# Kernel tuning notes

Hardware: AMD Instinct MI355X
Metric: run time of the kernel (lower is better)

Reference implementation:

```python
import jax, jax.numpy as jnp
import numpy as np

B, S, D, F, H, E = 2, 1024, 1024, 4096, 16, 8
EPS = 1e-5


def _layernorm(x, w, b):
    m = jnp.mean(x, -1, keepdims=True)
    v = jnp.var(x, -1, keepdims=True)
    return (x - m) * jax.lax.rsqrt(v + EPS) * w + b


def _rope(x):
    # rotary embedding applied over full embed dim (split-half convention)
    b, s, d = x.shape
    half = d // 2
    inv = 1.0 / (10000.0 ** (jnp.arange(half, dtype=jnp.float32) / half))
    ang = jnp.arange(s, dtype=jnp.float32)[:, None] * inv[None, :]  # [S, half]
    cos, sin = jnp.cos(ang), jnp.sin(ang)
    x1, x2 = x[..., :half], x[..., half:]
    return jnp.concatenate([x1 * cos - x2 * sin, x1 * sin + x2 * cos], -1)


def setup_inputs() -> dict:
    key = jax.random.key(0)
    ks = jax.random.split(key, 9)
    sc = 0.02
    return {
        "x": jax.random.normal(ks[0], (B, S, D), jnp.float32),
        "ln1_w": jnp.ones((D,), jnp.float32),
        "ln1_b": jnp.zeros((D,), jnp.float32),
        "ln2_w": jnp.ones((D,), jnp.float32),
        "ln2_b": jnp.zeros((D,), jnp.float32),
        "w_qkv": jax.random.normal(ks[1], (3 * D, D), jnp.float32) * sc,
        "b_qkv": jnp.zeros((3 * D,), jnp.float32),
        "w_out": jax.random.normal(ks[2], (D, D), jnp.float32) * sc,
        "b_out": jnp.zeros((D,), jnp.float32),
        "w_router": jax.random.normal(ks[3], (D, E), jnp.float32) * sc,
        "wi": jax.random.normal(ks[4], (E, D, F), jnp.float32) * sc,  # per-expert wi (no bias)
        "wo": jax.random.normal(ks[5], (E, F // 2, D), jnp.float32) * sc,  # swiglu halves ffn dim
    }


def reference(x, ln1_w, ln1_b, ln2_w, ln2_b, w_qkv, b_qkv, w_out, b_out, w_router, wi, wo):
    # ---- pre-norm self-attention block ----
    residual = x
    h = _layernorm(x, ln1_w, ln1_b)
    h = _rope(h)
    qkv = h @ w_qkv.T + b_qkv  # [B,S,3D]
    q, k, v = jnp.split(qkv, 3, axis=-1)
    hd = D // H
    to_heads = lambda t: t.reshape(B, S, H, hd).transpose(0, 2, 1, 3)
    q, k, v = to_heads(q), to_heads(k), to_heads(v)
    scale = 1.0 / np.sqrt(hd).astype(np.float32)
    att = jax.nn.softmax(jnp.einsum('bhqd,bhkd->bhqk', q, k) * scale, axis=-1)
    o = jnp.einsum('bhqk,bhkd->bhqd', att, v).transpose(0, 2, 1, 3).reshape(B, S, D)
    o = o @ w_out.T + b_out
    x = residual + o  # attn dropout is identity at eval

    # ---- pre-norm sparse MoE FFN block ----
    residual = x
    h = _layernorm(x, ln2_w, ln2_b)
    # top-1 router in float32
    logits = h.astype(jnp.float32) @ w_router  # [B,S,E]
    probs = jax.nn.softmax(logits, axis=-1)
    mask = jax.nn.one_hot(jnp.argmax(probs, -1), E, dtype=h.dtype)  # expert_mask
    gate = probs.astype(h.dtype) * mask  # router_probs * expert_mask, [B,S,E]
    # dense all-expert compute, masked combine (same math as gather/scatter loop)
    hid = jnp.einsum('bsd,edf->bsef', h, wi)  # [B,S,E,F]
    a, g = jnp.split(hid, 2, axis=-1)
    act = jax.nn.silu(a) * g  # SwiGLU, [B,S,E,F/2]
    y = jnp.einsum('bsef,efd,bse->bsd', act, wo, gate)
    x = residual + y
    return x, logits
```

## Files before the change

kernel.cpp:

```cpp
#include <hip/hip_runtime.h>
#include <hip/hip_bf16.h>
#include <math.h>

#define BB 2
#define SS 1024
#define DD 1024
#define FF 4096
#define HH 16
#define EE 8
#define MM (BB*SS)
#define MAX_TILES 24
#define MAX_TILES2 40

typedef __attribute__((ext_vector_type(8))) short bf16x8;
typedef __attribute__((ext_vector_type(8))) short s16x8;
typedef __attribute__((ext_vector_type(4))) float f32x4;

#define OFF_WIT  ((size_t)0)
#define OFF_WOT  ((size_t)67108864)
#define OFF_WQH  ((size_t)100663296)
#define OFF_WQL  ((size_t)106954752)
#define OFF_WOH  ((size_t)113246208)
#define OFF_WOL  ((size_t)115343360)
#define OFF_H1H  ((size_t)117440512)
#define OFF_H1L  ((size_t)121634816)
#define OFF_QKV  ((size_t)125829120)
#define OFF_OH   ((size_t)150994944)
#define OFF_OL   ((size_t)155189248)
#define OFF_X2   ((size_t)159383552)
#define OFF_H2B  ((size_t)167772160)
#define OFF_ACT  ((size_t)171966464)
#define OFF_GATE ((size_t)180879360)
#define OFF_EID  ((size_t)180887552)
#define OFF_PERM ((size_t)180895744)
#define OFF_CNT  ((size_t)180903936)
#define OFF_FILL ((size_t)180903968)
#define OFF_NT   ((size_t)180904000)
#define OFF_TE   ((size_t)180904192)
#define OFF_TS   ((size_t)180904320)
#define OFF_TR   ((size_t)180904448)
#define OFF_TE2  ((size_t)180904576)
#define OFF_TS2  ((size_t)180904768)
#define OFF_TR2  ((size_t)180904960)
#define OFF_NT2  ((size_t)180905152)
#define OFF_KSH  OFF_WQH
#define OFF_KSL  (OFF_WQH + 4194304)
#define OFF_VTH  OFF_H1H
#define OFF_VTL  OFF_H1L

__device__ __forceinline__ void gload16(const void* g, void* l) {
    __builtin_amdgcn_global_load_lds(
        (const __attribute__((address_space(1))) unsigned int*)g,
        (__attribute__((address_space(3))) unsigned int*)l, 16, 0, 0);
}

__device__ __forceinline__ short bfh(float v) {
    __hip_bfloat16 h = __float2bfloat16(v);
    return *(short*)&h;
}
__device__ __forceinline__ float bf2f(short s) {
    __hip_bfloat16 h = *(__hip_bfloat16*)&s;
    return __bfloat162float(h);
}

__device__ __forceinline__ void split_write(float v, __hip_bfloat16* hp, __hip_bfloat16* lp, size_t idx) {
    __hip_bfloat16 h = __float2bfloat16(v);
    hp[idx] = h;
    lp[idx] = __float2bfloat16(v - __bfloat162float(h));
}

__device__ __forceinline__ void tcvt64_body(const float* __restrict__ in, __hip_bfloat16* __restrict__ out,
                                            int R, int C, int r0, int c0, float* tile ) {
    int t = threadIdx.x;
    {
        int ri = t >> 2, cj = (t & 3) * 16;
        const float* ip = &in[(size_t)(r0 + ri) * C + c0 + cj];
#pragma unroll
        for (int k = 0; k < 4; ++k) {
            float4 v = *(const float4*)(ip + k * 4);
            tile[ri * 65 + cj + k * 4 + 0] = v.x;
            tile[ri * 65 + cj + k * 4 + 1] = v.y;
            tile[ri * 65 + cj + k * 4 + 2] = v.z;
            tile[ri * 65 + cj + k * 4 + 3] = v.w;
        }
    }
    __syncthreads();
    {
        int co = t >> 2, rj = (t & 3) * 16;
        bf16x8 v8a, v8b;
#pragma unroll
        for (int q = 0; q < 8; ++q) v8a[q] = bfh(tile[(rj + q) * 65 + co]);
#pragma unroll
        for (int q = 0; q < 8; ++q) v8b[q] = bfh(tile[(rj + 8 + q) * 65 + co]);
        __hip_bfloat16* op = &out[(size_t)(c0 + co) * R + r0 + rj];
        *(bf16x8*)op = v8a;
        *(bf16x8*)(op + 8) = v8b;
    }
}

__global__ void k_phase0(const float* __restrict__ x, const float* __restrict__ ln1w,
                         const float* __restrict__ ln1b,
                         __hip_bfloat16* __restrict__ h1H, __hip_bfloat16* __restrict__ h1L,
                         const float* __restrict__ w_qkv, __hip_bfloat16* __restrict__ wqH,
                         __hip_bfloat16* __restrict__ wqL,
                         const float* __restrict__ w_out, __hip_bfloat16* __restrict__ woH,
                         __hip_bfloat16* __restrict__ woL) {
    __shared__ __align__(16) float smem[1032];
    int bid = blockIdx.x, t = threadIdx.x;
    if (bid < 2048) {
        int m = bid, s = m & (SS - 1);
        float* row = smem;
        float* red = smem + 1024;
        const float* xp = x + (size_t)m * DD;
        float sum = 0.f, sumsq = 0.f;
#pragma unroll
        for (int l = 0; l < 4; ++l) {
            int i = t + l * 256;
            float v = xp[i];
            row[i] = v;
            sum += v; sumsq += v * v;
        }
#pragma unroll
        for (int off = 32; off; off >>= 1) {
            sum   += __shfl_xor(sum, off);
            sumsq += __shfl_xor(sumsq, off);
        }
        int wid = t >> 6, lane = t & 63;
        if (lane == 0) { red[wid] = sum; red[4 + wid] = sumsq; }
        __syncthreads();
        sum   = red[0] + red[1] + red[2] + red[3];
        sumsq = red[4] + red[5] + red[6] + red[7];
        float mean = sum * (1.f / DD);
        float var  = sumsq * (1.f / DD) - mean * mean;
        float rstd = rsqrtf(var + 1e-5f);
        size_t base = (size_t)m * DD;
        const float kln = logf(10000.f) / 512.f;
#pragma unroll
        for (int l = 0; l < 2; ++l) {
            int i = t + l * 256;
            float n1 = (row[i]       - mean) * rstd * ln1w[i]       + ln1b[i];
            float n2 = (row[i + 512] - mean) * rstd * ln1w[i + 512] + ln1b[i + 512];
            float inv = expf(-(float)i * kln);
            float ang = (float)s * inv;
            float c = cosf(ang), sn = sinf(ang);
            split_write(n1 * c - n2 * sn,  h1H, h1L, base + i);
            split_write(n1 * sn + n2 * c, h1H, h1L, base + i + 512);
        }
    } else if (bid < 5120) {
        int idx = (bid - 2048) * 256 + t;
        float4 v = ((const float4*)w_qkv)[idx];
        split_write(v.x, wqH, wqL, (size_t)idx * 4 + 0);
        split_write(v.y, wqH, wqL, (size_t)idx * 4 + 1);
        split_write(v.z, wqH, wqL, (size_t)idx * 4 + 2);
        split_write(v.w, wqH, wqL, (size_t)idx * 4 + 3);
    } else {
        int idx = (bid - 5120) * 256 + t;
        float4 v = ((const float4*)w_out)[idx];
        split_write(v.x, woH, woL, (size_t)idx * 4 + 0);
        split_write(v.y, woH, woL, (size_t)idx * 4 + 1);
        split_write(v.z, woH, woL, (size_t)idx * 4 + 2);
        split_write(v.w, woH, woL, (size_t)idx * 4 + 3);
    }
}

__global__ void k_qkv_mega(const __hip_bfloat16* __restrict__ Ah, const __hip_bfloat16* __restrict__ Al,
                           const __hip_bfloat16* __restrict__ Bh, const __hip_bfloat16* __restrict__ Bl,
                           const float* __restrict__ bias, float* __restrict__ Cf,
                           const float* __restrict__ wi, __hip_bfloat16* __restrict__ wiT) {
    __shared__ __align__(16) char smem[24576];
    int bid = blockIdx.x;
    const int t = threadIdx.x;
    if (bid < 768) {
        const int N = 3072, K = DD;
        short* AsH = (short*)smem;
        short* AsL = (short*)(smem + 4096);
        short* BsH = (short*)(smem + 8192);
        short* BsL = (short*)(smem + 16384);
        int m0 = (bid / 24) * 64, n0 = (bid % 24) * 128;
        const int w = t >> 6, lane = t & 63;
        const int sid = w * 64 + lane;
        const int g = lane >> 4, r16 = lane & 15;

        f32x4 acc[4][2] = {};

        for (int k0 = 0; k0 < K; k0 += 32) {
            {
                int rrow = sid >> 2, sl = sid & 3;
                int slog = sl ^ ((rrow >> 1) & 3);
                size_t lbase = (size_t)(w * 64) * 8;
                size_t gaoff = (size_t)(m0 + rrow) * K + k0 + slog * 8;
                gload16(Ah + gaoff, &AsH[lbase]);
                gload16(Al + gaoff, &AsL[lbase]);
            }
#pragma unroll
            for (int j = 0; j < 2; ++j) {
                int id = j * 256 + sid;
                int rrow = id >> 2, sl = id & 3;
                int slog = sl ^ ((rrow >> 1) & 3);
                size_t lbase = (size_t)(j * 256 + w * 64) * 8;
                size_t gboff = (size_t)(n0 + rrow) * K + k0 + slog * 8;
                gload16(Bh + gboff, &BsH[lbase]);
                gload16(Bl + gboff, &BsL[lbase]);
            }
            __syncthreads();
            bf16x8 ah[4], al[4], bh[2], bl[2];
#pragma unroll
            for (int i = 0; i < 4; ++i) {
                int ra = i * 16 + r16;
                int pa = g ^ ((ra >> 1) & 3);
                ah[i] = *(const bf16x8*)&AsH[ra * 32 + pa * 8];
                al[i] = *(const bf16x8*)&AsL[ra * 32 + pa * 8];
            }
#pragma unroll
            for (int n = 0; n < 2; ++n) {
                int rb = w * 32 + n * 16 + r16;
                int pb = g ^ ((rb >> 1) & 3);
                bh[n] = *(const bf16x8*)&BsH[rb * 32 + pb * 8];
                bl[n] = *(const bf16x8*)&BsL[rb * 32 + pb * 8];
            }
#pragma unroll
            for (int i = 0; i < 4; ++i)
#pragma unroll
                for (int n = 0; n < 2; ++n) {
                    acc[i][n] = __builtin_amdgcn_mfma_f32_16x16x32_bf16(ah[i], bh[n], acc[i][n], 0, 0, 0);
                    acc[i][n] = __builtin_amdgcn_mfma_f32_16x16x32_bf16(ah[i], bl[n], acc[i][n], 0, 0, 0);
                    acc[i][n] = __builtin_amdgcn_mfma_f32_16x16x32_bf16(al[i], bh[n], acc[i][n], 0, 0, 0);
                }
            __syncthreads();
        }

#pragma unroll
        for (int i = 0; i < 4; ++i) {
#pragma unroll
            for (int n = 0; n < 2; ++n) {
                int col = n0 + w * 32 + n * 16 + r16;
#pragma unroll
                for (int q = 0; q < 4; ++q) {
                    int r = m0 + i * 16 + g * 4 + q;
                    Cf[(size_t)r * N + col] = acc[i][n][q] + bias[col];
                }
            }
        }
    } else {
        int j = bid - 768;
        int e = j >> 10, rem = j & 1023;
        int ry = rem >> 6, cx = rem & 63;
        tcvt64_body(wi + (size_t)e * DD * FF, wiT + (size_t)e * DD * FF,
                    1024, 4096, ry * 64, cx * 64, (float*)smem);
    }
}

__global__ void k_oproj64(const __hip_bfloat16* __restrict__ Ah, const __hip_bfloat16* __restrict__ Al,
                          const __hip_bfloat16* __restrict__ Bh, const __hip_bfloat16* __restrict__ Bl,
                          const float* __restrict__ bias, const float* __restrict__ addsrc,
                          float* __restrict__ Cf, int* __restrict__ zero17) {
    __shared__ __align__(16) short AsH[64 * 32];
    __shared__ __align__(16) short AsL[64 * 32];
    __shared__ __align__(16) short BsH[128 * 32];
    __shared__ __align__(16) short BsL[128 * 32];
    const int N = DD, K = DD;
    int bid = blockIdx.x;
    int m0 = (bid >> 3) * 64, n0 = (bid & 7) * 128;
    const int t = threadIdx.x;
    if (bid == 0 && t < 17) zero17[t] = 0;
    const int w = t >> 6, lane = t & 63;
    const int sid = w * 64 + lane;
    const int g = lane >> 4, r16 = lane & 15;

    f32x4 acc[4][2] = {};

    for (int k0 = 0; k0 < K; k0 += 32) {
        {
            int rrow = sid >> 2, sl = sid & 3;
            int slog = sl ^ ((rrow >> 1) & 3);
            size_t lbase = (size_t)(w * 64) * 8;
            size_t gaoff = (size_t)(m0 + rrow) * K + k0 + slog * 8;
            gload16(Ah + gaoff, &AsH[lbase]);
            gload16(Al + gaoff, &AsL[lbase]);
        }
#pragma unroll
        for (int j = 0; j < 2; ++j) {
            int id = j * 256 + sid;
            int rrow = id >> 2, sl = id & 3;
            int slog = sl ^ ((rrow >> 1) & 3);
            size_t lbase = (size_t)(j * 256 + w * 64) * 8;
            size_t gboff = (size_t)(n0 + rrow) * K + k0 + slog * 8;
            gload16(Bh + gboff, &BsH[lbase]);
            gload16(Bl + gboff, &BsL[lbase]);
        }
        __syncthreads();
        bf16x8 ah[4], al[4], bh[2], bl[2];
#pragma unroll
        for (int i = 0; i < 4; ++i) {
            int ra = i * 16 + r16;
            int pa = g ^ ((ra >> 1) & 3);
            ah[i] = *(const bf16x8*)&AsH[ra * 32 + pa * 8];
            al[i] = *(const bf16x8*)&AsL[ra * 32 + pa * 8];
        }
#pragma unroll
        for (int n = 0; n < 2; ++n) {
            int rb = w * 32 + n * 16 + r16;
            int pb = g ^ ((rb >> 1) & 3);
            bh[n] = *(const bf16x8*)&BsH[rb * 32 + pb * 8];
            bl[n] = *(const bf16x8*)&BsL[rb * 32 + pb * 8];
        }
#pragma unroll
        for (int i = 0; i < 4; ++i)
#pragma unroll
            for (int n = 0; n < 2; ++n) {
                acc[i][n] = __builtin_amdgcn_mfma_f32_16x16x32_bf16(ah[i], bh[n], acc[i][n], 0, 0, 0);
                acc[i][n] = __builtin_amdgcn_mfma_f32_16x16x32_bf16(ah[i], bl[n], acc[i][n], 0, 0, 0);
                acc[i][n] = __builtin_amdgcn_mfma_f32_16x16x32_bf16(al[i], bh[n], acc[i][n], 0, 0, 0);
            }
        __syncthreads();
    }

#pragma unroll
    for (int i = 0; i < 4; ++i) {
#pragma unroll
        for (int n = 0; n < 2; ++n) {
            int col = n0 + w * 32 + n * 16 + r16;
#pragma unroll
            for (int q = 0; q < 4; ++q) {
                int r = m0 + i * 16 + g * 4 + q;
                Cf[(size_t)r * N + col] =
                    acc[i][n][q] + bias[col] + addsrc[(size_t)r * N + col];
            }
        }
    }
}

__global__ void k_moe_up(const __hip_bfloat16* __restrict__ A,
                         const __hip_bfloat16* __restrict__ Bt,
                         __hip_bfloat16* __restrict__ act,
                         const int* __restrict__ perm,
                         const int* __restrict__ te, const int* __restrict__ ts,
                         const int* __restrict__ tr, const int* __restrict__ ntl,
                         const float* __restrict__ wo, __hip_bfloat16* __restrict__ woT) {
    __shared__ __align__(16) char smem[17408];
    int bid = blockIdx.x;
    const int t = threadIdx.x;
    if (bid >= 768) {
        int j = bid - 768;
        int e = j >> 9, rem = j & 511;
        int ry = rem >> 4, cx = rem & 15;
        tcvt64_body(wo + (size_t)e * 2048 * 1024, woT + (size_t)e * 2048 * 1024,
                    2048, 1024, ry * 64, cx * 64, (float*)smem);
        return;
    }
    short* As = (short*)smem;
    short* Bs = (short*)(smem + 8192);
    int* permS = (int*)(smem + 16384);
    int tile = bid / 32;
    if (tile >= *ntl) return;
    int e = te[tile], rs = ts[tile], rows = tr[tile];
    if (t < 128) permS[t] = (t < rows) ? perm[rs + t] : 0;
    __syncthreads();
    int c0 = (bid & 31) * 64;
    const int w = t >> 6, lane = t & 63;
    const int wr = w >> 1, wc = w & 1;
    const int sid = w * 64 + lane;
    const int g = lane >> 4, r16 = lane & 15;

    const __hip_bfloat16* Bp = Bt + (size_t)e * FF * DD;

    f32x4 acc[4][4] = {};

    for (int k0 = 0; k0 < DD; k0 += 32) {
#pragma unroll
        for (int j = 0; j < 2; ++j) {
            int id = j * 256 + sid;
            int rrow = id >> 2, sl = id & 3;
            int slog = sl ^ ((rrow >> 1) & 3);
            size_t lbase = (size_t)(j * 256 + w * 64) * 8;
            gload16(A + (size_t)permS[rrow] * DD + k0 + slog * 8, &As[lbase]);
            int q = rrow >> 4, rr = rrow & 15;
            int wrow = c0 + (q >> 2) * 32 + ((q & 3) >> 1) * 16 + rr + (q & 1) * 2048;
            gload16(Bp + (size_t)wrow * DD + k0 + slog * 8, &Bs[lbase]);
        }
        __syncthreads();
        bf16x8 af[4], bfr[4];
#pragma unroll
        for (int i = 0; i < 4; ++i) {
            int ra = wr * 64 + i * 16 + r16;
            int pa = g ^ ((ra >> 1) & 3);
            af[i] = *(const bf16x8*)&As[ra * 32 + pa * 8];
            int rb = wc * 64 + i * 16 + r16;
            int pb = g ^ ((rb >> 1) & 3);
            bfr[i] = *(const bf16x8*)&Bs[rb * 32 + pb * 8];
        }
#pragma unroll
        for (int i = 0; i < 4; ++i)
#pragma unroll
            for (int n = 0; n < 4; ++n)
                acc[i][n] = __builtin_amdgcn_mfma_f32_16x16x32_bf16(af[i], bfr[n], acc[i][n], 0, 0, 0);
        __syncthreads();
    }

#pragma unroll
    for (int i = 0; i < 4; ++i) {
#pragma unroll
        for (int p2 = 0; p2 < 2; ++p2) {
            int col = c0 + wc * 32 + p2 * 16 + r16;
#pragma unroll
            for (int q = 0; q < 4; ++q) {
                int r = wr * 64 + i * 16 + g * 4 + q;
                if (r < rows) {
                    float a  = acc[i][2 * p2][q];
                    float gv = acc[i][2 * p2 + 1][q];
                    act[(size_t)(rs + r) * 2048 + col] =
                        __float2bfloat16((a / (1.f + expf(-a))) * gv);
                }
            }
        }
    }
}

__global__ void k_moe_dn(const __hip_bfloat16* __restrict__ A,
                         const __hip_bfloat16* __restrict__ Bt,
                         const float* __restrict__ addsrc, float* __restrict__ Cf,
                         const int* __restrict__ perm,
                         const int* __restrict__ te2, const int* __restrict__ ts2,
                         const int* __restrict__ tr2, const int* __restrict__ ntl2,
                         const float* __restrict__ gate) {
    __shared__ __align__(16) short As[64 * 32];
    __shared__ __align__(16) short Bs[128 * 32];
    __shared__ int permS[64];
    int tile = blockIdx.y;
    if (tile >= *ntl2) return;
    int e = te2[tile], rs = ts2[tile], rows = tr2[tile];
    const int t = threadIdx.x;
    if (t < 64) permS[t] = (t < rows) ? perm[rs + t] : 0;
    __syncthreads();
    int n0 = blockIdx.x * 128;
    const int w = t >> 6, lane = t & 63;
    const int sid = w * 64 + lane;
    const int g = lane >> 4, r16 = lane & 15;
    const int K = FF / 2;

    const __hip_bfloat16* Bp = Bt + (size_t)e * DD * (FF / 2);

    f32x4 acc[4][2] = {};

    for (int k0 = 0; k0 < K; k0 += 32) {
        {
            int rrow = sid >> 2, sl = sid & 3;
            int slog = sl ^ ((rrow >> 1) & 3);
            size_t lbase = (size_t)(w * 64) * 8;
            gload16(A + (size_t)(rs + rrow) * K + k0 + slog * 8, &As[lbase]);
        }
#pragma unroll
        for (int j = 0; j < 2; ++j) {
            int id = j * 256 + sid;
            int rrow = id >> 2, sl = id & 3;
            int slog = sl ^ ((rrow >> 1) & 3);
            size_t lbase = (size_t)(j * 256 + w * 64) * 8;
            gload16(Bp + (size_t)(n0 + rrow) * K + k0 + slog * 8, &Bs[lbase]);
        }
        __syncthreads();
        bf16x8 af[4], bfr[2];
#pragma unroll
        for (int i = 0; i < 4; ++i) {
            int ra = i * 16 + r16;
            int pa = g ^ ((ra >> 1) & 3);
            af[i] = *(const bf16x8*)&As[ra * 32 + pa * 8];
        }
#pragma unroll
        for (int n = 0; n < 2; ++n) {
            int rb = w * 32 + n * 16 + r16;
            int pb = g ^ ((rb >> 1) & 3);
            bfr[n] = *(const bf16x8*)&Bs[rb * 32 + pb * 8];
        }
#pragma unroll
        for (int i = 0; i < 4; ++i)
#pragma unroll
            for (int n = 0; n < 2; ++n)
                acc[i][n] = __builtin_amdgcn_mfma_f32_16x16x32_bf16(af[i], bfr[n], acc[i][n], 0, 0, 0);
        __syncthreads();
    }

#pragma unroll
    for (int i = 0; i < 4; ++i) {
#pragma unroll
        for (int n = 0; n < 2; ++n) {
            int col = n0 + w * 32 + n * 16 + r16;
#pragma unroll
            for (int q = 0; q < 4; ++q) {
                int r = i * 16 + g * 4 + q;
                if (r >= rows) continue;
                int tok = permS[r];
                Cf[(size_t)tok * DD + col] = addsrc[(size_t)tok * DD + col] + gate[tok] * acc[i][n][q];
            }
        }
    }
}

__global__ void k_prep(const float* __restrict__ qkv, short* __restrict__ KH, short* __restrict__ KL,
                       short* __restrict__ VH, short* __restrict__ VL) {
    __shared__ float tile[64][65];
    int b = blockIdx.z, h = blockIdx.y, s0 = blockIdx.x * 64;
    int t = threadIdx.x;
    int row = t >> 2, c0 = (t & 3) * 16;
    const float* kp = qkv + (size_t)(b * SS + s0 + row) * 3072 + 1024 + h * 64 + c0;
    const float* vp = kp + 1024;
    {
        size_t krow = ((size_t)(b * HH + h) * SS + s0 + row) * 64;
        int key = (s0 + row) & 7;
#pragma unroll
        for (int g2 = 0; g2 < 2; ++g2) {
            s16x8 hv, lv;
#pragma unroll
            for (int j = 0; j < 8; ++j) {
                float v = kp[g2 * 8 + j];
                short hh = bfh(v);
                hv[j] = hh; lv[j] = bfh(v - bf2f(hh));
            }
            int p = ((c0 >> 3) + g2) ^ key;
            *(s16x8*)&KH[krow + p * 8] = hv;
            *(s16x8*)&KL[krow + p * 8] = lv;
        }
    }
#pragma unroll
    for (int j = 0; j < 16; ++j) tile[row][c0 + j] = vp[j];
    __syncthreads();
    {
        int d = t >> 2, sc = (t & 3) * 16;
        size_t vrow = ((size_t)(b * HH + h) * 64 + d) * SS + s0;
        int key = d & 7;
#pragma unroll
        for (int g2 = 0; g2 < 2; ++g2) {
            s16x8 hv, lv;
#pragma unroll
            for (int j = 0; j < 8; ++j) {
                float v = tile[sc + g2 * 8 + j][d];
                short hh = bfh(v);
                hv[j] = hh; lv[j] = bfh(v - bf2f(hh));
            }
            int p = ((sc >> 3) + g2) ^ key;
            *(s16x8*)&VH[vrow + p * 8] = hv;
            *(s16x8*)&VL[vrow + p * 8] = lv;
        }
    }
}

#define LDP 72
__global__ __launch_bounds__(512, 4)
void k_attn_mfma(const float* __restrict__ qkv,
                 const short* __restrict__ KH, const short* __restrict__ KL,
                 const short* __restrict__ VH, const short* __restrict__ VL,
                 __hip_bfloat16* __restrict__ ohi, __hip_bfloat16* __restrict__ olo) {
    __shared__ __align__(16) short Ks[64 * 64], Kl2[64 * 64], Vs[64 * 64], Vl2[64 * 64];
    __shared__ __align__(16) short PhS[8][16 * LDP], PlS[8][16 * LDP];
    int id = blockIdx.x;
    int xcd = id & 7, slot = id >> 3;
    int bh = xcd * 4 + (slot >> 3);
    int q0 = (slot & 7) * 128;
    int b = bh >> 4, h = bh & 15;
    int t = threadIdx.x;
    int w = t >> 6, lane = t & 63;
    int g = lane >> 4, r16 = lane & 15;
    int srow = t >> 3, sslot = t & 7;

    const size_t kbase = ((size_t)bh * SS) * 64;
    const size_t vbase = ((size_t)bh * 64) * SS;

    bf16x8 qfh[2], qfl[2];
    {
        const float* qp = qkv + (size_t)(b * SS + q0 + w * 16 + r16) * 3072 + h * 64;
#pragma unroll
        for (int ks = 0; ks < 2; ++ks) {
            float vv[8];
            *(float4*)&vv[0] = *(const float4*)(qp + ks * 32 + g * 8);
            *(float4*)&vv[4] = *(const float4*)(qp + ks * 32 + g * 8 + 4);
#pragma unroll
            for (int j = 0; j < 8; ++j) {
                float sv = vv[j] * 0.125f;
                short hh = bfh(sv);
                qfh[ks][j] = hh;
                qfl[ks][j] = bfh(sv - bf2f(hh));
            }
        }
    }

    float mrun[4], lrun[4];
    f32x4 oacc[4] = {};
#pragma unroll
    for (int q = 0; q < 4; ++q) { mrun[q] = -1e30f; lrun[q] = 0.f; }

    for (int k0 = 0; k0 < SS; k0 += 64) {
        gload16(KH + kbase + (size_t)(k0 + srow) * 64 + sslot * 8, &Ks[w * 512]);
        gload16(KL + kbase + (size_t)(k0 + srow) * 64 + sslot * 8, &Kl2[w * 512]);
        gload16(VH + vbase + (size_t)srow * SS + k0 + sslot * 8,   &Vs[w * 512]);
        gload16(VL + vbase + (size_t)srow * SS + k0 + sslot * 8,   &Vl2[w * 512]);
        __syncthreads();

        f32x4 accs[4] = {};
#pragma unroll
        for (int ks = 0; ks < 2; ++ks) {
            bf16x8 kfh[4], kfl[4];
#pragma unroll
            for (int n = 0; n < 4; ++n) {
                int rb = n * 16 + r16;
                int p = (ks * 4 + g) ^ (r16 & 7);
                kfh[n] = *(const bf16x8*)&Ks[rb * 64 + p * 8];
                kfl[n] = *(const bf16x8*)&Kl2[rb * 64 + p * 8];
            }
            __builtin_amdgcn_s_setprio(1);
#pragma unroll
            for (int n = 0; n < 4; ++n) {
                accs[n] = __builtin_amdgcn_mfma_f32_16x16x32_bf16(qfh[ks], kfh[n], accs[n], 0, 0, 0);
                accs[n] = __builtin_amdgcn_mfma_f32_16x16x32_bf16(qfh[ks], kfl[n], accs[n], 0, 0, 0);
                accs[n] = __builtin_amdgcn_mfma_f32_16x16x32_bf16(qfl[ks], kfh[n], accs[n], 0, 0, 0);
            }
            __builtin_amdgcn_s_setprio(0);
        }

        float mn[4], corr[4], psum[4];
#pragma unroll
        for (int q = 0; q < 4; ++q) {
            float m = fmaxf(fmaxf(accs[0][q], accs[1][q]), fmaxf(accs[2][q], accs[3][q]));
            m = fmaxf(m, __shfl_xor(m, 1));
            m = fmaxf(m, __shfl_xor(m, 2));
            m = fmaxf(m, __shfl_xor(m, 4));
            m = fmaxf(m, __shfl_xor(m, 8));
            mn[q] = fmaxf(mrun[q], m);
            corr[q] = expf(mrun[q] - mn[q]);
            mrun[q] = mn[q];
            psum[q] = 0.f;
        }
#pragma unroll
        for (int n = 0; n < 4; ++n)
#pragma unroll
            for (int q = 0; q < 4; ++q) {
                float p = expf(accs[n][q] - mn[q]);
                psum[q] += p;
                short ph = bfh(p);
                PhS[w][(g * 4 + q) * LDP + n * 16 + r16] = ph;
                PlS[w][(g * 4 + q) * LDP + n * 16 + r16] = bfh(p - bf2f(ph));
            }
#pragma unroll
        for (int q = 0; q < 4; ++q) {
            psum[q] += __shfl_xor(psum[q], 1);
            psum[q] += __shfl_xor(psum[q], 2);
            psum[q] += __shfl_xor(psum[q], 4);
            psum[q] += __shfl_xor(psum[q], 8);
            lrun[q] = lrun[q] * corr[q] + psum[q];
#pragma unroll
            for (int n = 0; n < 4; ++n) oacc[n][q] *= corr[q];
        }

#pragma unroll
        for (int ks = 0; ks < 2; ++ks) {
            bf16x8 vfh[4], vfl[4];
#pragma unroll
            for (int n = 0; n < 4; ++n) {
                int rb = n * 16 + r16;
                int p = (ks * 4 + g) ^ (r16 & 7);
                vfh[n] = *(const bf16x8*)&Vs[rb * 64 + p * 8];
                vfl[n] = *(const bf16x8*)&Vl2[rb * 64 + p * 8];
            }
            bf16x8 pfh = *(const bf16x8*)&PhS[w][r16 * LDP + ks * 32 + g * 8];
            bf16x8 pfl = *(const bf16x8*)&PlS[w][r16 * LDP + ks * 32 + g * 8];
            __builtin_amdgcn_s_setprio(1);
#pragma unroll
            for (int n = 0; n < 4; ++n) {
                oacc[n] = __builtin_amdgcn_mfma_f32_16x16x32_bf16(pfh, vfh[n], oacc[n], 0, 0, 0);
                oacc[n] = __builtin_amdgcn_mfma_f32_16x16x32_bf16(pfh, vfl[n], oacc[n], 0, 0, 0);
                oacc[n] = __builtin_amdgcn_mfma_f32_16x16x32_bf16(pfl, vfh[n], oacc[n], 0, 0, 0);
            }
            __builtin_amdgcn_s_setprio(0);
        }
        __syncthreads();
    }

    float invl[4];
#pragma unroll
    for (int q = 0; q < 4; ++q) invl[q] = 1.f / lrun[q];
#pragma unroll
    for (int n = 0; n < 4; ++n) {
        int col = h * 64 + n * 16 + r16;
#pragma unroll
        for (int q = 0; q < 4; ++q) {
            int rowg = b * SS + q0 + w * 16 + g * 4 + q;
            split_write(oacc[n][q] * invl[q], ohi, olo, (size_t)rowg * DD + col);
        }
    }
}

__global__ void k_ln2_router(const float* __restrict__ x2, const float* __restrict__ w,
                             const float* __restrict__ b, const float* __restrict__ wr,
                             __hip_bfloat16* __restrict__ h2b, float* __restrict__ logits,
                             float* __restrict__ gate, int* __restrict__ eid,
                             int* __restrict__ counts) {
    int m = blockIdx.x, t = threadIdx.x;
    __shared__ float red[8];
    __shared__ float racc[4][8];
    const float* xp = x2 + (size_t)m * DD;
    float v[4];
    float sum = 0.f, sumsq = 0.f;
#pragma unroll
    for (int l = 0; l < 4; ++l) {
        v[l] = xp[t + l * 256];
        sum += v[l]; sumsq += v[l] * v[l];
    }
#pragma unroll
    for (int off = 32; off; off >>= 1) {
        sum   += __shfl_xor(sum, off);
        sumsq += __shfl_xor(sumsq, off);
    }
    int wid = t >> 6, lane = t & 63;
    if (lane == 0) { red[wid] = sum; red[4 + wid] = sumsq; }
    __syncthreads();
    sum   = red[0] + red[1] + red[2] + red[3];
    sumsq = red[4] + red[5] + red[6] + red[7];
    float mean = sum * (1.f / DD);
    float var  = sumsq * (1.f / DD) - mean * mean;
    float rstd = rsqrtf(var + 1e-5f);
    float acc[EE] = {};
#pragma unroll
    for (int l = 0; l < 4; ++l) {
        int i = t + l * 256;
        float hv = (v[l] - mean) * rstd * w[i] + b[i];
        h2b[(size_t)m * DD + i] = __float2bfloat16(hv);
        const float* wp = wr + (size_t)i * EE;
#pragma unroll
        for (int n = 0; n < EE; ++n) acc[n] += hv * wp[n];
    }
#pragma unroll
    for (int off = 32; off; off >>= 1)
#pragma unroll
        for (int n = 0; n < EE; ++n) acc[n] += __shfl_xor(acc[n], off);
    if (lane == 0)
#pragma unroll
        for (int n = 0; n < EE; ++n) racc[wid][n] = acc[n];
    __syncthreads();
    if (t == 0) {
        float lg[EE];
#pragma unroll
        for (int n = 0; n < EE; ++n) lg[n] = racc[0][n] + racc[1][n] + racc[2][n] + racc[3][n];
        float mx = lg[0]; int best = 0;
#pragma unroll
        for (int n = 1; n < EE; ++n) if (lg[n] > mx) { mx = lg[n]; best = n; }
        float den = 0.f;
#pragma unroll
        for (int n = 0; n < EE; ++n) den += expf(lg[n] - mx);
        gate[m] = 1.f / den;
        eid[m] = best;
        atomicAdd(&counts[best], 1);
#pragma unroll
        for (int n = 0; n < EE; ++n) logits[(size_t)m * EE + n] = lg[n];
    }
}

__global__ void k_offscatter(const int* __restrict__ counts,
                             int* __restrict__ te, int* __restrict__ ts, int* __restrict__ tr,
                             int* __restrict__ ntl,
                             int* __restrict__ te2, int* __restrict__ ts2, int* __restrict__ tr2,
                             int* __restrict__ ntl2,
                             const int* __restrict__ eid,
                             int* __restrict__ fill, int* __restrict__ perm) {
    __shared__ int soffs[EE];
    int t = threadIdx.x;
    if (t == 0) {
        int off = 0, nt = 0, nt2 = 0;
        for (int e = 0; e < EE; ++e) {
            soffs[e] = off;
            int c = counts[e];
            for (int t0 = 0; t0 < c; t0 += 128) {
                te[nt] = e; ts[nt] = off + t0; tr[nt] = (c - t0 < 128) ? (c - t0) : 128; ++nt;
            }
            for (int t0 = 0; t0 < c; t0 += 64) {
                te2[nt2] = e; ts2[nt2] = off + t0; tr2[nt2] = (c - t0 < 64) ? (c - t0) : 64; ++nt2;
            }
            off += c;
        }
        *ntl = nt;
        *ntl2 = nt2;
    }
    __syncthreads();
#pragma unroll
    for (int tok = t; tok < MM; tok += 1024) {
        int e = eid[tok];
        int pos = soffs[e] + atomicAdd(&fill[e], 1);
        perm[pos] = tok;
    }
}

extern "C" void kernel_launch(void* const* d_in, const int* in_sizes, int n_in,
                              void* d_out, int out_size, void* d_ws, size_t ws_size,
                              hipStream_t stream) {
    const float* x     = (const float*)d_in[0];
    const float* ln1w  = (const float*)d_in[1];
    const float* ln1b  = (const float*)d_in[2];
    const float* ln2w  = (const float*)d_in[3];
    const float* ln2b  = (const float*)d_in[4];
    const float* w_qkv = (const float*)d_in[5];
    const float* b_qkv = (const float*)d_in[6];
    const float* w_out = (const float*)d_in[7];
    const float* b_out = (const float*)d_in[8];
    const float* w_rtr = (const float*)d_in[9];
    const float* wi    = (const float*)d_in[10];
    const float* wo    = (const float*)d_in[11];
    float* out = (float*)d_out;

    char* wsb = (char*)d_ws;
    __hip_bfloat16* wiT  = (__hip_bfloat16*)(wsb + OFF_WIT);
    __hip_bfloat16* woT  = (__hip_bfloat16*)(wsb + OFF_WOT);
    __hip_bfloat16* wqH  = (__hip_bfloat16*)(wsb + OFF_WQH);
    __hip_bfloat16* wqL  = (__hip_bfloat16*)(wsb + OFF_WQL);
    __hip_bfloat16* woH  = (__hip_bfloat16*)(wsb + OFF_WOH);
    __hip_bfloat16* woL  = (__hip_bfloat16*)(wsb + OFF_WOL);
    __hip_bfloat16* h1H  = (__hip_bfloat16*)(wsb + OFF_H1H);
    __hip_bfloat16* h1L  = (__hip_bfloat16*)(wsb + OFF_H1L);
    float*          qkvF = (float*)(wsb + OFF_QKV);
    __hip_bfloat16* oH   = (__hip_bfloat16*)(wsb + OFF_OH);
    __hip_bfloat16* oL   = (__hip_bfloat16*)(wsb + OFF_OL);
    float*          x2F  = (float*)(wsb + OFF_X2);
    __hip_bfloat16* h2B  = (__hip_bfloat16*)(wsb + OFF_H2B);
    __hip_bfloat16* actB = (__hip_bfloat16*)(wsb + OFF_ACT);
    short* KSH = (short*)(wsb + OFF_KSH);
    short* KSL = (short*)(wsb + OFF_KSL);
    short* VTH = (short*)(wsb + OFF_VTH);
    short* VTL = (short*)(wsb + OFF_VTL);
    float* gate = (float*)(wsb + OFF_GATE);
    int* eid    = (int*)(wsb + OFF_EID);
    int* perm   = (int*)(wsb + OFF_PERM);
    int* counts = (int*)(wsb + OFF_CNT);
    int* fill   = (int*)(wsb + OFF_FILL);
    int* ntl    = (int*)(wsb + OFF_NT);
    int* te     = (int*)(wsb + OFF_TE);
    int* tsx    = (int*)(wsb + OFF_TS);
    int* trx    = (int*)(wsb + OFF_TR);
    int* te2    = (int*)(wsb + OFF_TE2);
    int* ts2    = (int*)(wsb + OFF_TS2);
    int* tr2    = (int*)(wsb + OFF_TR2);
    int* ntl2   = (int*)(wsb + OFF_NT2);

    k_phase0<<<6144, 256, 0, stream>>>(x, ln1w, ln1b, h1H, h1L, w_qkv, wqH, wqL,
                                       w_out, woH, woL);
    k_qkv_mega<<<8960, 256, 0, stream>>>(h1H, h1L, wqH, wqL, b_qkv, qkvF, wi, wiT);
    k_prep<<<dim3(SS / 64, HH, BB), 256, 0, stream>>>(qkvF, KSH, KSL, VTH, VTL);
    k_attn_mfma<<<256, 512, 0, stream>>>(qkvF, KSH, KSL, VTH, VTL, oH, oL);
    k_oproj64<<<256, 256, 0, stream>>>(oH, oL, woH, woL, b_out, x, x2F, counts);
    k_ln2_router<<<MM, 256, 0, stream>>>(x2F, ln2w, ln2b, w_rtr, h2B,
                                         out + (size_t)MM * DD, gate, eid, counts);
    k_offscatter<<<1, 1024, 0, stream>>>(counts, te, tsx, trx, ntl,
                                         te2, ts2, tr2, ntl2, eid, fill, perm);
    k_moe_up<<<768 + 4096, 256, 0, stream>>>(h2B, wiT, actB, perm, te, tsx, trx, ntl,
                                             wo, woT);
    k_moe_dn<<<dim3(DD / 128, MAX_TILES2), 256, 0, stream>>>(
        actB, woT, x2F, out, perm, te2, ts2, tr2, ntl2, gate);
}
```

Measured before the change: 320.3 us.

## Move expert weight transposes into attention kernel and XCD-swizzle QKV GEMM

The wi and wo transpose-to-bf16 blocks move out of the QKV GEMM and MoE-up kernels and become extra blocks of the attention kernel, two 256-thread tiles per 512-thread block. The attention kernel is only 256 blocks, so the transpose work is meant to fill idle CUs alongside it. The QKV GEMM becomes a plain 768-block kernel whose tile mapping groups N tiles per XCD for L2 reuse. In exchange, attention now reserves a larger shared buffer (68 KB), which may lower its occupancy.

```diff
diff --git a/kernel.cpp b/kernel.cpp
--- a/kernel.cpp
+++ b/kernel.cpp
@@ -70,8 +70,7 @@
 }
 
 __device__ __forceinline__ void tcvt64_body(const float* __restrict__ in, __hip_bfloat16* __restrict__ out,
-                                            int R, int C, int r0, int c0, float* tile ) {
-    int t = threadIdx.x;
+                                            int R, int C, int r0, int c0, float* tile , int t) {
     {
         int ri = t >> 2, cj = (t & 3) * 16;
         const float* ip = &in[(size_t)(r0 + ri) * C + c0 + cj];
@@ -163,90 +162,83 @@
     }
 }
 
-__global__ void k_qkv_mega(const __hip_bfloat16* __restrict__ Ah, const __hip_bfloat16* __restrict__ Al,
-                           const __hip_bfloat16* __restrict__ Bh, const __hip_bfloat16* __restrict__ Bl,
-                           const float* __restrict__ bias, float* __restrict__ Cf,
-                           const float* __restrict__ wi, __hip_bfloat16* __restrict__ wiT) {
-    __shared__ __align__(16) char smem[24576];
+__global__ void k_qkv(const __hip_bfloat16* __restrict__ Ah, const __hip_bfloat16* __restrict__ Al,
+                      const __hip_bfloat16* __restrict__ Bh, const __hip_bfloat16* __restrict__ Bl,
+                      const float* __restrict__ bias, float* __restrict__ Cf) {
+    __shared__ __align__(16) short AsH[64 * 32];
+    __shared__ __align__(16) short AsL[64 * 32];
+    __shared__ __align__(16) short BsH[128 * 32];
+    __shared__ __align__(16) short BsL[128 * 32];
+    const int N = 3072, K = DD;
     int bid = blockIdx.x;
+    int xcd = bid & 7, idx = bid >> 3;
+    int nt = xcd + (idx >> 5) * 8;
+    int mt = idx & 31;
+    int m0 = mt * 64, n0 = nt * 128;
     const int t = threadIdx.x;
-    if (bid < 768) {
-        const int N = 3072, K = DD;
-        short* AsH = (short*)smem;
-        short* AsL = (short*)(smem + 4096);
-        short* BsH = (short*)(smem + 8192);
-        short* BsL = (short*)(smem + 16384);
-        int m0 = (bid / 24) * 64, n0 = (bid % 24) * 128;
-        const int w = t >> 6, lane = t & 63;
-        const int sid = w * 64 + lane;
-        const int g = lane >> 4, r16 = lane & 15;
-
-        f32x4 acc[4][2] = {};
-
-        for (int k0 = 0; k0 < K; k0 += 32) {
-            {
-                int rrow = sid >> 2, sl = sid & 3;
-                int slog = sl ^ ((rrow >> 1) & 3);
-                size_t lbase = (size_t)(w * 64) * 8;
-                size_t gaoff = (size_t)(m0 + rrow) * K + k0 + slog * 8;
-                gload16(Ah + gaoff, &AsH[lbase]);
-                gload16(Al + gaoff, &AsL[lbase]);
-            }
-#pragma unroll
-            for (int j = 0; j < 2; ++j) {
-                int id = j * 256 + sid;
-                int rrow = id >> 2, sl = id & 3;
-                int slog = sl ^ ((rrow >> 1) & 3);
-                size_t lbase = (size_t)(j * 256 + w * 64) * 8;
-                size_t gboff = (size_t)(n0 + rrow) * K + k0 + slog * 8;
-                gload16(Bh + gboff, &BsH[lbase]);
-                gload16(Bl + gboff, &BsL[lbase]);
-            }
-            __syncthreads();
-            bf16x8 ah[4], al[4], bh[2], bl[2];
-#pragma unroll
-            for (int i = 0; i < 4; ++i) {
-                int ra = i * 16 + r16;
-                int pa = g ^ ((ra >> 1) & 3);
-                ah[i] = *(const bf16x8*)&AsH[ra * 32 + pa * 8];
-                al[i] = *(const bf16x8*)&AsL[ra * 32 + pa * 8];
-            }
+    const int w = t >> 6, lane = t & 63;
+    const int sid = w * 64 + lane;
+    const int g = lane >> 4, r16 = lane & 15;
+
+    f32x4 acc[4][2] = {};
+
+    for (int k0 = 0; k0 < K; k0 += 32) {
+        {
+            int rrow = sid >> 2, sl = sid & 3;
+            int slog = sl ^ ((rrow >> 1) & 3);
+            size_t lbase = (size_t)(w * 64) * 8;
+            size_t gaoff = (size_t)(m0 + rrow) * K + k0 + slog * 8;
+            gload16(Ah + gaoff, &AsH[lbase]);
+            gload16(Al + gaoff, &AsL[lbase]);
+        }
+#pragma unroll
+        for (int j = 0; j < 2; ++j) {
+            int id = j * 256 + sid;
+            int rrow = id >> 2, sl = id & 3;
+            int slog = sl ^ ((rrow >> 1) & 3);
+            size_t lbase = (size_t)(j * 256 + w * 64) * 8;
+            size_t gboff = (size_t)(n0 + rrow) * K + k0 + slog * 8;
+            gload16(Bh + gboff, &BsH[lbase]);
+            gload16(Bl + gboff, &BsL[lbase]);
+        }
+        __syncthreads();
+        bf16x8 ah[4], al[4], bh[2], bl[2];
+#pragma unroll
+        for (int i = 0; i < 4; ++i) {
+            int ra = i * 16 + r16;
+            int pa = g ^ ((ra >> 1) & 3);
+            ah[i] = *(const bf16x8*)&AsH[ra * 32 + pa * 8];
+            al[i] = *(const bf16x8*)&AsL[ra * 32 + pa * 8];
+        }
+#pragma unroll
+        for (int n = 0; n < 2; ++n) {
+            int rb = w * 32 + n * 16 + r16;
+            int pb = g ^ ((rb >> 1) & 3);
+            bh[n] = *(const bf16x8*)&BsH[rb * 32 + pb * 8];
+            bl[n] = *(const bf16x8*)&BsL[rb * 32 + pb * 8];
+        }
+#pragma unroll
+        for (int i = 0; i < 4; ++i)
 #pragma unroll
             for (int n = 0; n < 2; ++n) {
-                int rb = w * 32 + n * 16 + r16;
-                int pb = g ^ ((rb >> 1) & 3);
-                bh[n] = *(const bf16x8*)&BsH[rb * 32 + pb * 8];
-                bl[n] = *(const bf16x8*)&BsL[rb * 32 + pb * 8];
-            }
-#pragma unroll
-            for (int i = 0; i < 4; ++i)
-#pragma unroll
-                for (int n = 0; n < 2; ++n) {
-                    acc[i][n] = __builtin_amdgcn_mfma_f32_16x16x32_bf16(ah[i], bh[n], acc[i][n], 0, 0, 0);
-                    acc[i][n] = __builtin_amdgcn_mfma_f32_16x16x32_bf16(ah[i], bl[n], acc[i][n], 0, 0, 0);
-                    acc[i][n] = __builtin_amdgcn_mfma_f32_16x16x32_bf16(al[i], bh[n], acc[i][n], 0, 0, 0);
-                }
-            __syncthreads();
-        }
-
-#pragma unroll
-        for (int i = 0; i < 4; ++i) {
-#pragma unroll
-            for (int n = 0; n < 2; ++n) {
-                int col = n0 + w * 32 + n * 16 + r16;
-#pragma unroll
-                for (int q = 0; q < 4; ++q) {
-                    int r = m0 + i * 16 + g * 4 + q;
-                    Cf[(size_t)r * N + col] = acc[i][n][q] + bias[col];
-                }
-            }
-        }
-    } else {
-        int j = bid - 768;
-        int e = j >> 10, rem = j & 1023;
-        int ry = rem >> 6, cx = rem & 63;
-        tcvt64_body(wi + (size_t)e * DD * FF, wiT + (size_t)e * DD * FF,
-                    1024, 4096, ry * 64, cx * 64, (float*)smem);
+                acc[i][n] = __builtin_amdgcn_mfma_f32_16x16x32_bf16(ah[i], bh[n], acc[i][n], 0, 0, 0);
+                acc[i][n] = __builtin_amdgcn_mfma_f32_16x16x32_bf16(ah[i], bl[n], acc[i][n], 0, 0, 0);
+                acc[i][n] = __builtin_amdgcn_mfma_f32_16x16x32_bf16(al[i], bh[n], acc[i][n], 0, 0, 0);
+            }
+        __syncthreads();
+    }
+
+#pragma unroll
+    for (int i = 0; i < 4; ++i) {
+#pragma unroll
+        for (int n = 0; n < 2; ++n) {
+            int col = n0 + w * 32 + n * 16 + r16;
+#pragma unroll
+            for (int q = 0; q < 4; ++q) {
+                int r = m0 + i * 16 + g * 4 + q;
+                Cf[(size_t)r * N + col] = acc[i][n][q] + bias[col];
+            }
+        }
     }
 }
 
@@ -335,28 +327,17 @@
                          __hip_bfloat16* __restrict__ act,
                          const int* __restrict__ perm,
                          const int* __restrict__ te, const int* __restrict__ ts,
-                         const int* __restrict__ tr, const int* __restrict__ ntl,
-                         const float* __restrict__ wo, __hip_bfloat16* __restrict__ woT) {
-    __shared__ __align__(16) char smem[17408];
-    int bid = blockIdx.x;
-    const int t = threadIdx.x;
-    if (bid >= 768) {
-        int j = bid - 768;
-        int e = j >> 9, rem = j & 511;
-        int ry = rem >> 4, cx = rem & 15;
-        tcvt64_body(wo + (size_t)e * 2048 * 1024, woT + (size_t)e * 2048 * 1024,
-                    2048, 1024, ry * 64, cx * 64, (float*)smem);
-        return;
-    }
-    short* As = (short*)smem;
-    short* Bs = (short*)(smem + 8192);
-    int* permS = (int*)(smem + 16384);
-    int tile = bid / 32;
+                         const int* __restrict__ tr, const int* __restrict__ ntl) {
+    __shared__ __align__(16) short As[128 * 32];
+    __shared__ __align__(16) short Bs[128 * 32];
+    __shared__ int permS[128];
+    int tile = blockIdx.y;
     if (tile >= *ntl) return;
     int e = te[tile], rs = ts[tile], rows = tr[tile];
+    const int t = threadIdx.x;
     if (t < 128) permS[t] = (t < rows) ? perm[rs + t] : 0;
     __syncthreads();
-    int c0 = (bid & 31) * 64;
+    int c0 = blockIdx.x * 64;
     const int w = t >> 6, lane = t & 63;
     const int wr = w >> 1, wc = w & 1;
     const int sid = w * 64 + lane;
@@ -545,13 +526,38 @@
 
 #define LDP 72
 __global__ __launch_bounds__(512, 4)
-void k_attn_mfma(const float* __restrict__ qkv,
+void k_attn_mega(const float* __restrict__ qkv,
                  const short* __restrict__ KH, const short* __restrict__ KL,
                  const short* __restrict__ VH, const short* __restrict__ VL,
-                 __hip_bfloat16* __restrict__ ohi, __hip_bfloat16* __restrict__ olo) {
-    __shared__ __align__(16) short Ks[64 * 64], Kl2[64 * 64], Vs[64 * 64], Vl2[64 * 64];
-    __shared__ __align__(16) short PhS[8][16 * LDP], PlS[8][16 * LDP];
+                 __hip_bfloat16* __restrict__ ohi, __hip_bfloat16* __restrict__ olo,
+                 const float* __restrict__ wi, __hip_bfloat16* __restrict__ wiT,
+                 const float* __restrict__ wo, __hip_bfloat16* __restrict__ woT) {
+    __shared__ __align__(16) char smem[69632];
     int id = blockIdx.x;
+    if (id >= 256) {
+        int t512 = threadIdx.x;
+        int half = t512 >> 8, t = t512 & 255;
+        float* tile = (float*)(smem + half * 33280 / 2 * 2);
+        tile = (float*)(smem + half * 16640);
+        if (id < 4352) {
+            int gidx = (id - 256) * 2 + half;
+            int e = gidx >> 10, rem = gidx & 1023;
+            int ry = rem >> 6, cx = rem & 63;
+            tcvt64_body(wi + (size_t)e * DD * FF, wiT + (size_t)e * DD * FF,
+                        1024, 4096, ry * 64, cx * 64, tile, t);
+        } else {
+            int gidx = (id - 4352) * 2 + half;
+            int e = gidx >> 9, rem = gidx & 511;
+            int ry = rem >> 4, cx = rem & 15;
+            tcvt64_body(wo + (size_t)e * 2048 * 1024, woT + (size_t)e * 2048 * 1024,
+                        2048, 1024, ry * 64, cx * 64, tile, t);
+        }
+        return;
+    }
+    short* Ks  = (short*)smem;
+    short* Kl2 = (short*)(smem + 8192);
+    short* Vs  = (short*)(smem + 16384);
+    short* Vl2 = (short*)(smem + 24576);
     int xcd = id & 7, slot = id >> 3;
     int bh = xcd * 4 + (slot >> 3);
     int q0 = (slot & 7) * 128;
@@ -560,6 +566,8 @@
     int w = t >> 6, lane = t & 63;
     int g = lane >> 4, r16 = lane & 15;
     int srow = t >> 3, sslot = t & 7;
+    short* PhS = (short*)(smem + 32768 + w * 2304);
+    short* PlS = (short*)(smem + 51200 + w * 2304);
 
     const size_t kbase = ((size_t)bh * SS) * 64;
     const size_t vbase = ((size_t)bh * 64) * SS;
@@ -588,10 +596,10 @@
     for (int q = 0; q < 4; ++q) { mrun[q] = -1e30f; lrun[q] = 0.f; }
 
     for (int k0 = 0; k0 < SS; k0 += 64) {
-        gload16(KH + kbase + (size_t)(k0 + srow) * 64 + sslot * 8, &Ks[w * 512]);
-        gload16(KL + kbase + (size_t)(k0 + srow) * 64 + sslot * 8, &Kl2[w * 512]);
-        gload16(VH + vbase + (size_t)srow * SS + k0 + sslot * 8,   &Vs[w * 512]);
-        gload16(VL + vbase + (size_t)srow * SS + k0 + sslot * 8,   &Vl2[w * 512]);
+        gload16(KH + kbase + (size_t)(k0 + srow) * 64 + sslot * 8, Ks  + w * 512);
+        gload16(KL + kbase + (size_t)(k0 + srow) * 64 + sslot * 8, Kl2 + w * 512);
+        gload16(VH + vbase + (size_t)srow * SS + k0 + sslot * 8,   Vs  + w * 512);
+        gload16(VL + vbase + (size_t)srow * SS + k0 + sslot * 8,   Vl2 + w * 512);
         __syncthreads();
 
         f32x4 accs[4] = {};
@@ -635,8 +643,8 @@
                 float p = expf(accs[n][q] - mn[q]);
                 psum[q] += p;
                 short ph = bfh(p);
-                PhS[w][(g * 4 + q) * LDP + n * 16 + r16] = ph;
-                PlS[w][(g * 4 + q) * LDP + n * 16 + r16] = bfh(p - bf2f(ph));
+                PhS[(g * 4 + q) * LDP + n * 16 + r16] = ph;
+                PlS[(g * 4 + q) * LDP + n * 16 + r16] = bfh(p - bf2f(ph));
             }
 #pragma unroll
         for (int q = 0; q < 4; ++q) {
@@ -659,8 +667,8 @@
                 vfh[n] = *(const bf16x8*)&Vs[rb * 64 + p * 8];
                 vfl[n] = *(const bf16x8*)&Vl2[rb * 64 + p * 8];
             }
-            bf16x8 pfh = *(const bf16x8*)&PhS[w][r16 * LDP + ks * 32 + g * 8];
-            bf16x8 pfl = *(const bf16x8*)&PlS[w][r16 * LDP + ks * 32 + g * 8];
+            bf16x8 pfh = *(const bf16x8*)&PhS[r16 * LDP + ks * 32 + g * 8];
+            bf16x8 pfl = *(const bf16x8*)&PlS[r16 * LDP + ks * 32 + g * 8];
             __builtin_amdgcn_s_setprio(1);
 #pragma unroll
             for (int n = 0; n < 4; ++n) {
@@ -838,16 +846,16 @@
 
     k_phase0<<<6144, 256, 0, stream>>>(x, ln1w, ln1b, h1H, h1L, w_qkv, wqH, wqL,
                                        w_out, woH, woL);
-    k_qkv_mega<<<8960, 256, 0, stream>>>(h1H, h1L, wqH, wqL, b_qkv, qkvF, wi, wiT);
+    k_qkv<<<768, 256, 0, stream>>>(h1H, h1L, wqH, wqL, b_qkv, qkvF);
     k_prep<<<dim3(SS / 64, HH, BB), 256, 0, stream>>>(qkvF, KSH, KSL, VTH, VTL);
-    k_attn_mfma<<<256, 512, 0, stream>>>(qkvF, KSH, KSL, VTH, VTL, oH, oL);
+    k_attn_mega<<<6400, 512, 0, stream>>>(qkvF, KSH, KSL, VTH, VTL, oH, oL,
+                                          wi, wiT, wo, woT);
     k_oproj64<<<256, 256, 0, stream>>>(oH, oL, woH, woL, b_out, x, x2F, counts);
     k_ln2_router<<<MM, 256, 0, stream>>>(x2F, ln2w, ln2b, w_rtr, h2B,
                                          out + (size_t)MM * DD, gate, eid, counts);
     k_offscatter<<<1, 1024, 0, stream>>>(counts, te, tsx, trx, ntl,
                                          te2, ts2, tr2, ntl2, eid, fill, perm);
-    k_moe_up<<<768 + 4096, 256, 0, stream>>>(h2B, wiT, actB, perm, te, tsx, trx, ntl,
-                                             wo, woT);
+    k_moe_up<<<dim3(32, MAX_TILES), 256, 0, stream>>>(h2B, wiT, actB, perm, te, tsx, trx, ntl);
     k_moe_dn<<<dim3(DD / 128, MAX_TILES2), 256, 0, stream>>>(
         actB, woT, x2F, out, perm, te2, ts2, tr2, ntl2, gate);
 }
```

New measurement: 307.0 us. -4.2%, faster.
